# Optimization experiments

Measured on AMD Instinct MI355X. Metric: run time of the kernel, lower is better.

## Reference

```python
import jax, jax.numpy as jnp
import numpy as np

N = 50000      # nodes
E = 800000     # edges
FIN = 128      # num_feature
EDIM = 16      # edge_dim
OUT = 64       # out_dim (per-head channels; concat=False averages heads)
H = 4          # heads
SCALE = 1.0 / float(np.sqrt(OUT))


def _layernorm(h, g, b):
    mu = h.mean(-1, keepdims=True)
    var = ((h - mu) ** 2).mean(-1, keepdims=True)
    return (h - mu) * jax.lax.rsqrt(var + 1e-5) * g + b


def _tconv(x, src, dst, ea, Wq, bq, Wk, bk, Wv, bv, We, Ws, bs):
    # PyG TransformerConv, concat=False, root_weight=True, eval mode (no dropout)
    n = x.shape[0]
    q = (x @ Wq + bq).reshape(n, H, OUT)[dst]   # [E,H,D] query at destination
    k = (x @ Wk + bk).reshape(n, H, OUT)[src]   # [E,H,D] key at source
    v = (x @ Wv + bv).reshape(n, H, OUT)[src]   # [E,H,D] value at source
    e = (ea @ We).reshape(-1, H, OUT)           # [E,H,D] edge embedding (no bias)
    logits = jnp.einsum('ehd,ehd->eh', q, k + e) * SCALE   # [E,H]
    # segment softmax over incoming edges of each destination node
    m = jax.lax.stop_gradient(jax.ops.segment_max(logits, dst, num_segments=n))
    a = jnp.exp(logits - m[dst])
    s = jax.ops.segment_sum(a, dst, num_segments=n)
    alpha = a / s[dst]                                     # [E,H]
    agg = jax.ops.segment_sum((v + e) * alpha[..., None], dst, num_segments=n)  # [N,H,D]
    return agg.mean(axis=1) + x @ Ws + bs      # concat=False -> head mean; + skip


def _forward(x, src, dst, ea, p1, p2, p3, g, b):
    h = x
    for p in (p1, p2, p3):
        h = jax.nn.gelu(_layernorm(_tconv(h, src, dst, ea, *p), g, b), approximate=False)
    return h


def setup_inputs() -> dict:
    key = jax.random.key(0)
    ks = iter(jax.random.split(key, 64))
    def nrm(shp, s=0.05):
        return jax.random.normal(next(ks), shp, jnp.float32) * s
    inp = {
        'x': nrm((N, FIN), 1.0),
        'edge_index': jax.random.randint(next(ks), (2, E), 0, N),
        'edge_attr': nrm((E, EDIM), 1.0),
    }
    for l, fin in ((1, FIN), (2, OUT), (3, OUT)):
        inp[f'Wq{l}'] = nrm((fin, H * OUT)); inp[f'bq{l}'] = jnp.zeros((H * OUT,), jnp.float32)
        inp[f'Wk{l}'] = nrm((fin, H * OUT)); inp[f'bk{l}'] = jnp.zeros((H * OUT,), jnp.float32)
        inp[f'Wv{l}'] = nrm((fin, H * OUT)); inp[f'bv{l}'] = jnp.zeros((H * OUT,), jnp.float32)
        inp[f'We{l}'] = nrm((EDIM, H * OUT))
        inp[f'Ws{l}'] = nrm((fin, OUT)); inp[f'bs{l}'] = jnp.zeros((OUT,), jnp.float32)
    inp['ln_g'] = jnp.ones((OUT,), jnp.float32)
    inp['ln_b'] = jnp.zeros((OUT,), jnp.float32)
    return inp


def reference(x, edge_index, edge_attr,
              Wq1, bq1, Wk1, bk1, Wv1, bv1, We1, Ws1, bs1,
              Wq2, bq2, Wk2, bk2, Wv2, bv2, We2, Ws2, bs2,
              Wq3, bq3, Wk3, bk3, Wv3, bv3, We3, Ws3, bs3,
              ln_g, ln_b):
    src, dst = edge_index[0], edge_index[1]
    p1 = (Wq1, bq1, Wk1, bk1, Wv1, bv1, We1, Ws1, bs1)
    p2 = (Wq2, bq2, Wk2, bk2, Wv2, bv2, We2, Ws2, bs2)
    p3 = (Wq3, bq3, Wk3, bk3, Wv3, bv3, We3, Ws3, bs3)
    return _forward(x, src, dst, edge_attr, p1, p2, p3, ln_g, ln_b)
```

## Files before the change

### kernel.cpp

```cpp
#include <hip/hip_runtime.h>
#include <hip/hip_bf16.h>
#include <math.h>

#define NNODES 50000
#define NEDGES 800000
#define HD     256
#define CW     384
#define NTOT   896
#define QS     0.18033688011112042f

typedef __hip_bfloat16 bf16;
typedef unsigned short u16;
typedef unsigned char  u8;
typedef unsigned int   u32;
typedef __attribute__((ext_vector_type(8))) short bf16x8;
typedef __attribute__((ext_vector_type(4))) float f32x4;
typedef __attribute__((ext_vector_type(2))) float f32x2;

__device__ __forceinline__ float lo16f(u32 u) { return __uint_as_float(u << 16); }
__device__ __forceinline__ float hi16f(u32 u) { return __uint_as_float(u & 0xFFFF0000u); }
__device__ __forceinline__ short f2s(float v) { __hip_bfloat16 h = __float2bfloat16(v); return *(short*)&h; }

__device__ __forceinline__ void gload_lds16(const void* g, void* l) {
    __builtin_amdgcn_global_load_lds(
        (const __attribute__((address_space(1))) void*)g,
        (__attribute__((address_space(3))) void*)l, 16, 0, 0);
}

template<int CTRL>
__device__ __forceinline__ float dppadd(float x) {
    int t = __builtin_amdgcn_update_dpp(0, __float_as_int(x), CTRL, 0xF, 0xF, true);
    return x + __int_as_float(t);
}

__global__ void hist_kernel(const int* __restrict__ dst, int* __restrict__ deg, int E) {
    int e = blockIdx.x * 256 + threadIdx.x;
    if (e < E) atomicAdd(&deg[dst[e]], 1);
}

__global__ void scanA(const int* __restrict__ deg, int* __restrict__ locincl,
                      int* __restrict__ blocksum, int n) {
    int tid = threadIdx.x;
    int i = blockIdx.x * 256 + tid;
    int v = (i < n) ? deg[i] : 0;
    int lane = tid & 63, w = tid >> 6;
    int s = v;
    #pragma unroll
    for (int off = 1; off < 64; off <<= 1) {
        int t = __shfl_up(s, off);
        if (lane >= off) s += t;
    }
    __shared__ int wsum[4];
    if (lane == 63) wsum[w] = s;
    __syncthreads();
    for (int ww = 0; ww < w; ww++) s += wsum[ww];
    if (i < n) locincl[i] = s;
    if (tid == 255) blocksum[blockIdx.x] = s;
}

__global__ void scanB(const int* __restrict__ blocksum, int* __restrict__ blockoff,
                      int nb, int* __restrict__ rowptr, int n) {
    int tid = threadIdx.x;
    int v = (tid < nb) ? blocksum[tid] : 0;
    int lane = tid & 63, w = tid >> 6;
    int s = v;
    #pragma unroll
    for (int off = 1; off < 64; off <<= 1) {
        int t = __shfl_up(s, off);
        if (lane >= off) s += t;
    }
    __shared__ int wsum[4];
    if (lane == 63) wsum[w] = s;
    __syncthreads();
    for (int ww = 0; ww < w; ww++) s += wsum[ww];
    if (tid < nb) blockoff[tid] = s - v;
    if (tid == 255) rowptr[n] = s;
}

__global__ void scanC(const int* __restrict__ deg, const int* __restrict__ locincl,
                      const int* __restrict__ blockoff,
                      int* __restrict__ rowptr, int* __restrict__ cursor, int n) {
    int i = blockIdx.x * 256 + threadIdx.x;
    if (i < n) {
        int ex = locincl[i] - deg[i] + blockoff[blockIdx.x];
        rowptr[i] = ex;
        cursor[i] = ex;
    }
}

__global__ void scatter_kernel(const int* __restrict__ src, const int* __restrict__ dst,
                               int* __restrict__ cursor,
                               int* __restrict__ csr_src, int* __restrict__ csr_eid, int E) {
    int e = blockIdx.x * 256 + threadIdx.x;
    if (e < E) {
        int d = dst[e];
        int p = atomicAdd(&cursor[d], 1);
        csr_src[p] = src[e];
        csr_eid[p] = e;
    }
}

__global__ void eperm(const int* __restrict__ csr_eid, const float* __restrict__ eattr,
                      u16* __restrict__ eattr_c) {
    int g = blockIdx.x * 256 + threadIdx.x;
    int p = g >> 2, part = g & 3;
    int eid = csr_eid[p];
    float4 v = *(const float4*)((const u8*)eattr + (size_t)eid * 64 + part * 16);
    union { u16 s[4]; uint2 u; } t;
    t.s[0] = (u16)f2s(v.x); t.s[1] = (u16)f2s(v.y); t.s[2] = (u16)f2s(v.z); t.s[3] = (u16)f2s(v.w);
    *(uint2*)((u8*)eattr_c + (size_t)p * 32 + part * 8) = t.u;
}

__global__ void xcast(const float* __restrict__ x, u16* __restrict__ xb) {
    int i = blockIdx.x * 256 + threadIdx.x;
    const float4* p = (const float4*)(x + (size_t)i * 8);
    float4 a = p[0], b = p[1];
    union { u16 s[8]; uint4 u; } t;
    t.s[0] = (u16)f2s(a.x); t.s[1] = (u16)f2s(a.y); t.s[2] = (u16)f2s(a.z); t.s[3] = (u16)f2s(a.w);
    t.s[4] = (u16)f2s(b.x); t.s[5] = (u16)f2s(b.y); t.s[6] = (u16)f2s(b.z); t.s[7] = (u16)f2s(b.w);
    *(uint4*)(xb + (size_t)i * 8) = t.u;
}

__global__ void pack_all(const float* __restrict__ Wq, const float* __restrict__ bq,
                         const float* __restrict__ Wk, const float* __restrict__ bk,
                         const float* __restrict__ Wv, const float* __restrict__ bv,
                         const float* __restrict__ We,
                         const float* __restrict__ Ws, const float* __restrict__ bs,
                         bf16* __restrict__ Wc, float* __restrict__ b, int K) {
    int n = blockIdx.x, c = threadIdx.x;
    float v, bb;
    if (n < 256)      { v = Wq[(size_t)c * 256 + n] * QS;    bb = bq[n] * QS; }
    else if (n < 320) {
        int t = n - 256, h = t >> 4, j = t & 15;
        float s = 0.f, sb = 0.f;
        #pragma unroll 8
        for (int d = 0; d < 64; d++) {
            float wv = We[j * HD + h * 64 + d];
            s += Wq[(size_t)c * 256 + h * 64 + d] * wv;
            sb += bq[h * 64 + d] * wv;
        }
        v = s * QS; bb = sb * QS;
    }
    else if (n < 384) { v = Ws[(size_t)c * 64  + (n - 320)]; bb = bs[n - 320]; }
    else if (n < 640) { v = Wv[(size_t)c * 256 + (n - 384)]; bb = bv[n - 384]; }
    else              { v = Wk[(size_t)c * 256 + (n - 640)]; bb = bk[n - 640]; }
    Wc[(size_t)n * K + c] = __float2bfloat16(v);
    if (c == 0) b[n] = bb;
}

template<int K>
__global__ void __launch_bounds__(256) gemm_v4(
    const u16* __restrict__ A, const bf16* __restrict__ Wc, const float* __restrict__ bias,
    bf16* __restrict__ comb, u8* __restrict__ kv)
{
    constexpr int KS    = K / 32;
    constexpr int ITERS = 4;
    constexpr int ROWB  = K * 2;
    constexpr int TILEB = 64 * ROWB;
    constexpr int WSEG  = TILEB / 4;
    constexpr int NINST = WSEG / 1024;
    __shared__ __align__(16) u8 Ab[2][TILEB];
    __shared__ __align__(16) u8 TrB[4][2560];
    int tid = threadIdx.x, w = tid >> 6, lane = tid & 63;
    int cl = lane & 15, aq = lane >> 4;
    int chunk = blockIdx.x;
    int slab = blockIdx.y * (64 * ITERS);
    u8* myT = TrB[w];

    bf16x8 bfr[4][KS];
    #pragma unroll
    for (int t = 0; t < 4; t++)
        #pragma unroll
        for (int ks = 0; ks < KS; ks++)
            bfr[t][ks] = *(const bf16x8*)((const u16*)Wc +
                         (size_t)(chunk * 64 + t * 16 + cl) * K + ks * 32 + aq * 8);

    float4 bv[4];
    #pragma unroll
    for (int t = 0; t < 4; t++) bv[t] = *(const float4*)&bias[chunk * 64 + t * 16 + aq * 4];

    auto STAGE = [&](int b, int it) {
        int m0 = slab + it * 64;
        #pragma unroll
        for (int i = 0; i < NINST; i++) {
            int off = w * WSEG + i * 1024;
            int rowbase = off / ROWB;
            int row, gran;
            if constexpr (K == 64) { row = rowbase + (lane >> 3); gran = lane & 7;  }
            else                   { row = rowbase + (lane >> 4); gran = lane & 15; }
            int gr = m0 + row; if (gr >= NNODES) gr = NNODES - 1;
            int sg = gran ^ (row & 7);
            gload_lds16((const u8*)A + (size_t)gr * ROWB + sg * 16, Ab[b] + off);
        }
    };

    STAGE(0, 0);
    __syncthreads();
    int cur = 0;
    #pragma unroll
    for (int it = 0; it < ITERS; it++) {
        if (it + 1 < ITERS) STAGE(cur ^ 1, it + 1);

        int rowt = w * 16 + cl;
        bf16x8 a[KS];
        #pragma unroll
        for (int ks = 0; ks < KS; ks++)
            a[ks] = *(const bf16x8*)&Ab[cur][rowt * ROWB + (((ks * 4 + aq) ^ (rowt & 7)) << 4)];

        f32x4 acc[4] = {};
        #pragma unroll
        for (int t = 0; t < 4; t++)
            #pragma unroll
            for (int ks = 0; ks < KS; ks++)
                acc[t] = __builtin_amdgcn_mfma_f32_16x16x32_bf16(bfr[t][ks], a[ks], acc[t], 0, 0, 0);

        if (chunk < 10) {
            #pragma unroll
            for (int t = 0; t < 4; t++) {
                u32 lo = (u32)(u16)f2s(acc[t][0] + bv[t].x) | ((u32)(u16)f2s(acc[t][1] + bv[t].y) << 16);
                u32 hi = (u32)(u16)f2s(acc[t][2] + bv[t].z) | ((u32)(u16)f2s(acc[t][3] + bv[t].w) << 16);
                *(uint2*)(myT + cl * 160 + t * 32 + aq * 8) = make_uint2(lo, hi);
            }
            #pragma unroll
            for (int i = 0; i < 2; i++) {
                int r = i * 8 + (lane >> 3);
                uint4 vv = *(const uint4*)(myT + r * 160 + (lane & 7) * 16);
                int gr = slab + it * 64 + w * 16 + r;
                if (gr < NNODES) {
                    u8* dst = (chunk < 6) ? (u8*)comb + (size_t)gr * (CW * 2) + chunk * 128
                                          : kv + (size_t)gr * 768 + (chunk - 6) * 128;
                    *(uint4*)(dst + (lane & 7) * 16) = vv;
                }
            }
        } else {
            #pragma unroll
            for (int t = 0; t < 4; t++) {
                u32 pk = __builtin_amdgcn_cvt_pk_fp8_f32(acc[t][0] + bv[t].x, acc[t][1] + bv[t].y, 0, false);
                pk = __builtin_amdgcn_cvt_pk_fp8_f32(acc[t][2] + bv[t].z, acc[t][3] + bv[t].w, pk, true);
                *(u32*)(myT + cl * 80 + (t * 4 + aq) * 4) = pk;
            }
            {
                int r = lane >> 2;
                uint4 vv = *(const uint4*)(myT + r * 80 + (lane & 3) * 16);
                int gr = slab + it * 64 + w * 16 + r;
                if (gr < NNODES)
                    *(uint4*)(kv + (size_t)gr * 768 + 512 + (chunk - 10) * 64 + (lane & 3) * 16) = vv;
            }
        }
        __syncthreads();
        cur ^= 1;
    }
}

__global__ void __launch_bounds__(256) node_fused(
    const int* __restrict__ rowptr, const int* __restrict__ csr_src,
    const u16* __restrict__ eattr_c, const u16* __restrict__ comb,
    const u8* __restrict__ kv,
    const float* __restrict__ We, const float* __restrict__ lng, const float* __restrict__ lnb,
    bf16* __restrict__ outB, float* __restrict__ outF)
{
    int tid = threadIdx.x, w = tid >> 6, lane = tid & 63;
    int n = blockIdx.x * 4 + w;
    int hg = lane >> 4, j16 = lane & 15, coff = 4 * lane;
    __shared__ float sAV[4][256];
    __shared__ float sAE[4][64];

    const u16* crow = comb + (size_t)n * CW;
    uint2 qv = *(const uint2*)(crow + coff);
    float qf0 = lo16f(qv.x), qf1 = hi16f(qv.x), qf2 = lo16f(qv.y), qf3 = hi16f(qv.y);
    float qwe_r = __uint_as_float((u32)crow[256 + lane] << 16);

    int e0 = __builtin_amdgcn_readfirstlane(rowptr[n]);
    int e1 = __builtin_amdgcn_readfirstlane(rowptr[n + 1]);

    float ss = 0.f, av0 = 0.f, av1 = 0.f, av2 = 0.f, av3 = 0.f, ae = 0.f;
    u32 vo = (u32)coff * 2u;
    u32 eo = (u32)j16 * 2u;

    auto EDGE = [&](int sm, int pos) {
        u32 s = (u32)__builtin_amdgcn_readfirstlane(sm);
        const u8* kvp = kv + (size_t)s * 768u;
        uint2 vw = *(const uint2*)(kvp + vo);
        u32   kw = *(const u32*)  (kvp + 512u + (u32)coff);
        float ea = lo16f((u32)*(const u16*)((const u8*)eattr_c + (size_t)(u32)pos * 32u + eo));
        f32x2 k01 = __builtin_amdgcn_cvt_pk_f32_fp8(kw, false);
        f32x2 k23 = __builtin_amdgcn_cvt_pk_f32_fp8(kw, true);
        float part = qf0 * k01[0] + qf1 * k01[1] + qf2 * k23[0] + qf3 * k23[1] + qwe_r * ea;
        part = dppadd<0xB1>(part);
        part = dppadd<0x4E>(part);
        part = dppadd<0x141>(part);
        part = dppadd<0x140>(part);
        float alpha = __builtin_amdgcn_exp2f(part);
        ss += alpha;
        ae += alpha * ea;
        av0 += alpha * lo16f(vw.x); av1 += alpha * hi16f(vw.x);
        av2 += alpha * lo16f(vw.y); av3 += alpha * hi16f(vw.y);
    };

    const int* cs = csr_src;
    int i = e0;
    int m0 = 0, m1 = 0, m2 = 0, m3 = 0, m4 = 0, m5 = 0, m6 = 0, m7 = 0;
    if (i + 7 < e1) {
        m0 = cs[i];     m1 = cs[i + 1]; m2 = cs[i + 2]; m3 = cs[i + 3];
        m4 = cs[i + 4]; m5 = cs[i + 5]; m6 = cs[i + 6]; m7 = cs[i + 7];
    }
    for (; i + 15 < e1; i += 8) {
        int n0 = cs[i + 8],  n1 = cs[i + 9],  n2 = cs[i + 10], n3 = cs[i + 11];
        int n4 = cs[i + 12], n5 = cs[i + 13], n6 = cs[i + 14], n7 = cs[i + 15];
        EDGE(m0, i);     EDGE(m1, i + 1); EDGE(m2, i + 2); EDGE(m3, i + 3);
        EDGE(m4, i + 4); EDGE(m5, i + 5); EDGE(m6, i + 6); EDGE(m7, i + 7);
        m0 = n0; m1 = n1; m2 = n2; m3 = n3; m4 = n4; m5 = n5; m6 = n6; m7 = n7;
    }
    if (i + 7 < e1) {
        EDGE(m0, i);     EDGE(m1, i + 1); EDGE(m2, i + 2); EDGE(m3, i + 3);
        EDGE(m4, i + 4); EDGE(m5, i + 5); EDGE(m6, i + 6); EDGE(m7, i + 7);
        i += 8;
    }
    for (; i < e1; ++i) EDGE(cs[i], i);

    float inv = (ss > 0.f) ? 1.f / ss : 0.f;
    *(float4*)&sAV[w][coff] = make_float4(av0 * inv, av1 * inv, av2 * inv, av3 * inv);
    sAE[w][lane] = ae * inv;

    int d = lane;
    float val = 0.f;
    #pragma unroll
    for (int h = 0; h < 4; h++) {
        float xv = sAV[w][h * 64 + d];
        #pragma unroll
        for (int j = 0; j < 16; j++) xv += sAE[w][h * 16 + j] * We[j * HD + h * 64 + d];
        val += xv;
    }
    val = val * 0.25f + __uint_as_float((u32)crow[320 + d] << 16);

    float m = val;
    #pragma unroll
    for (int off = 1; off < 64; off <<= 1) m += __shfl_xor(m, off);
    m *= (1.f / 64.f);
    float diff = val - m;
    float vr = diff * diff;
    #pragma unroll
    for (int off = 1; off < 64; off <<= 1) vr += __shfl_xor(vr, off);
    vr *= (1.f / 64.f);
    float y = diff * rsqrtf(vr + 1e-5f) * lng[d] + lnb[d];
    float ge = 0.5f * y * (1.f + erff(y * 0.70710678118654752f));
    if (outF) outF[(size_t)n * 64 + d] = ge;
    else      outB[(size_t)n * 64 + d] = __float2bfloat16(ge);
}

extern "C" void kernel_launch(void* const* d_in, const int* in_sizes, int n_in,
                              void* d_out, int out_size, void* d_ws, size_t ws_size,
                              hipStream_t stream)
{
    const float* x     = (const float*)d_in[0];
    const int*   eidx  = (const int*)d_in[1];
    const float* eattr = (const float*)d_in[2];
    struct P { const float *Wq,*bq,*Wk,*bk,*Wv,*bv,*We,*Ws,*bs; };
    P p[3];
    for (int l = 0; l < 3; l++) {
        int base = 3 + l * 9;
        p[l].Wq = (const float*)d_in[base + 0]; p[l].bq = (const float*)d_in[base + 1];
        p[l].Wk = (const float*)d_in[base + 2]; p[l].bk = (const float*)d_in[base + 3];
        p[l].Wv = (const float*)d_in[base + 4]; p[l].bv = (const float*)d_in[base + 5];
        p[l].We = (const float*)d_in[base + 6];
        p[l].Ws = (const float*)d_in[base + 7]; p[l].bs = (const float*)d_in[base + 8];
    }
    const float* lng = (const float*)d_in[30];
    const float* lnb = (const float*)d_in[31];

    char* ws = (char*)d_ws;
    size_t off = 0;
    auto alloc = [&](size_t bytes) { void* pp = ws + off; off += (bytes + 255) & ~(size_t)255; return pp; };
    int*   rowptr   = (int*)  alloc((NNODES + 1) * 4);
    int*   cursor   = (int*)  alloc(NNODES * 4);
    int*   deg      = (int*)  alloc(NNODES * 4);
    int*   blocksum = (int*)  alloc(256 * 4);
    int*   blockoff = (int*)  alloc(256 * 4);
    int*   csr_src  = (int*)  alloc((size_t)NEDGES * 4);
    int*   csr_eid  = (int*)  alloc((size_t)NEDGES * 4);
    u16*   eattr_c  = (u16*)  alloc((size_t)NEDGES * 16 * 2);
    bf16*  hbuf     = (bf16*) alloc((size_t)NNODES * 64 * 2);
    u16*   xb       = (u16*)  alloc((size_t)NNODES * 128 * 2);
    bf16*  comb     = (bf16*) alloc((size_t)NNODES * CW * 2);
    u8*    kv       = (u8*)   alloc((size_t)NNODES * 768);
    bf16*  Wc       = (bf16*) alloc((size_t)NTOT * 128 * 2);
    float* b896     = (float*)alloc(NTOT * 4);
    (void)ws_size;

    const int* srcArr = eidx;
    const int* dstArr = eidx + NEDGES;

    int NB = (NNODES + 255) / 256;
    (void)hipMemsetAsync(deg, 0, NNODES * 4, stream);
    hist_kernel<<<(NEDGES + 255) / 256, 256, 0, stream>>>(dstArr, deg, NEDGES);
    scanA<<<NB, 256, 0, stream>>>(deg, cursor, blocksum, NNODES);
    scanB<<<1, 256, 0, stream>>>(blocksum, blockoff, NB, rowptr, NNODES);
    scanC<<<NB, 256, 0, stream>>>(deg, cursor, blockoff, rowptr, cursor, NNODES);
    scatter_kernel<<<(NEDGES + 255) / 256, 256, 0, stream>>>(srcArr, dstArr, cursor, csr_src, csr_eid, NEDGES);
    eperm<<<(4 * NEDGES) / 256, 256, 0, stream>>>(csr_eid, eattr, eattr_c);
    xcast<<<(NNODES * 128 / 8 + 255) / 256, 256, 0, stream>>>(x, xb);

    int NBY = (NNODES + 255) / 256;
    int fins[3] = {128, 64, 64};

    const u16* hin = xb;
    for (int l = 0; l < 3; l++) {
        int FIN = fins[l];
        pack_all<<<NTOT, FIN, 0, stream>>>(p[l].Wq, p[l].bq, p[l].Wk, p[l].bk,
                                           p[l].Wv, p[l].bv, p[l].We, p[l].Ws, p[l].bs,
                                           Wc, b896, FIN);
        if (l == 0) gemm_v4<128><<<dim3(14, NBY), 256, 0, stream>>>(hin, Wc, b896, comb, kv);
        else        gemm_v4<64> <<<dim3(14, NBY), 256, 0, stream>>>(hin, Wc, b896, comb, kv);
        node_fused<<<NNODES / 4, 256, 0, stream>>>(rowptr, csr_src, eattr_c, (const u16*)comb,
            kv, p[l].We, lng, lnb,
            (l == 2) ? nullptr : hbuf, (l == 2) ? (float*)d_out : nullptr);
        hin = (const u16*)hbuf;
    }
}
```

Measured before the change: 662.1 us.

## Use persistent dynamic node scheduling and fuse edge-attr permute into scatter

The node aggregation kernel becomes a persistent grid of 2048 blocks whose waves claim pairs of nodes from a global atomic counter, one counter per layer, instead of one wave per node from a static grid. This is meant to balance the irregular per-node degree and cut wave launch overhead. Separately, the eperm kernel and the csr_eid buffer are removed: the scatter kernel now converts each edge's attributes to bf16 and writes them straight to their CSR slot. That saves a launch and an index round trip, but each thread now does a 32-byte scattered write, and the work queue adds atomic contention.

Result: slower. 1.560 ms (+135.6%).

```diff
diff --git a/kernel.cpp b/kernel.cpp
--- a/kernel.cpp
+++ b/kernel.cpp
@@ -89,26 +89,24 @@
 }
 
 __global__ void scatter_kernel(const int* __restrict__ src, const int* __restrict__ dst,
-                               int* __restrict__ cursor,
-                               int* __restrict__ csr_src, int* __restrict__ csr_eid, int E) {
+                               int* __restrict__ cursor, int* __restrict__ csr_src,
+                               const float* __restrict__ eattr, u16* __restrict__ eattr_c, int E) {
     int e = blockIdx.x * 256 + threadIdx.x;
     if (e < E) {
         int d = dst[e];
         int p = atomicAdd(&cursor[d], 1);
         csr_src[p] = src[e];
-        csr_eid[p] = e;
-    }
-}
-
-__global__ void eperm(const int* __restrict__ csr_eid, const float* __restrict__ eattr,
-                      u16* __restrict__ eattr_c) {
-    int g = blockIdx.x * 256 + threadIdx.x;
-    int p = g >> 2, part = g & 3;
-    int eid = csr_eid[p];
-    float4 v = *(const float4*)((const u8*)eattr + (size_t)eid * 64 + part * 16);
-    union { u16 s[4]; uint2 u; } t;
-    t.s[0] = (u16)f2s(v.x); t.s[1] = (u16)f2s(v.y); t.s[2] = (u16)f2s(v.z); t.s[3] = (u16)f2s(v.w);
-    *(uint2*)((u8*)eattr_c + (size_t)p * 32 + part * 8) = t.u;
+        const float4* er = (const float4*)(eattr + (size_t)e * 16);
+        float4 a = er[0], b = er[1], c = er[2], f = er[3];
+        union { u16 s[16]; uint4 u[2]; } t;
+        t.s[0]  = (u16)f2s(a.x); t.s[1]  = (u16)f2s(a.y); t.s[2]  = (u16)f2s(a.z); t.s[3]  = (u16)f2s(a.w);
+        t.s[4]  = (u16)f2s(b.x); t.s[5]  = (u16)f2s(b.y); t.s[6]  = (u16)f2s(b.z); t.s[7]  = (u16)f2s(b.w);
+        t.s[8]  = (u16)f2s(c.x); t.s[9]  = (u16)f2s(c.y); t.s[10] = (u16)f2s(c.z); t.s[11] = (u16)f2s(c.w);
+        t.s[12] = (u16)f2s(f.x); t.s[13] = (u16)f2s(f.y); t.s[14] = (u16)f2s(f.z); t.s[15] = (u16)f2s(f.w);
+        uint4* dstp = (uint4*)((u8*)eattr_c + (size_t)p * 32);
+        dstp[0] = t.u[0];
+        dstp[1] = t.u[1];
+    }
 }
 
 __global__ void xcast(const float* __restrict__ x, u16* __restrict__ xb) {
@@ -253,6 +251,7 @@
 }
 
 __global__ void __launch_bounds__(256) node_fused(
+    int* __restrict__ ctr,
     const int* __restrict__ rowptr, const int* __restrict__ csr_src,
     const u16* __restrict__ eattr_c, const u16* __restrict__ comb,
     const u8* __restrict__ kv,
@@ -260,92 +259,102 @@
     bf16* __restrict__ outB, float* __restrict__ outF)
 {
     int tid = threadIdx.x, w = tid >> 6, lane = tid & 63;
-    int n = blockIdx.x * 4 + w;
     int hg = lane >> 4, j16 = lane & 15, coff = 4 * lane;
     __shared__ float sAV[4][256];
     __shared__ float sAE[4][64];
 
-    const u16* crow = comb + (size_t)n * CW;
-    uint2 qv = *(const uint2*)(crow + coff);
-    float qf0 = lo16f(qv.x), qf1 = hi16f(qv.x), qf2 = lo16f(qv.y), qf3 = hi16f(qv.y);
-    float qwe_r = __uint_as_float((u32)crow[256 + lane] << 16);
-
-    int e0 = __builtin_amdgcn_readfirstlane(rowptr[n]);
-    int e1 = __builtin_amdgcn_readfirstlane(rowptr[n + 1]);
-
-    float ss = 0.f, av0 = 0.f, av1 = 0.f, av2 = 0.f, av3 = 0.f, ae = 0.f;
     u32 vo = (u32)coff * 2u;
     u32 eo = (u32)j16 * 2u;
-
-    auto EDGE = [&](int sm, int pos) {
-        u32 s = (u32)__builtin_amdgcn_readfirstlane(sm);
-        const u8* kvp = kv + (size_t)s * 768u;
-        uint2 vw = *(const uint2*)(kvp + vo);
-        u32   kw = *(const u32*)  (kvp + 512u + (u32)coff);
-        float ea = lo16f((u32)*(const u16*)((const u8*)eattr_c + (size_t)(u32)pos * 32u + eo));
-        f32x2 k01 = __builtin_amdgcn_cvt_pk_f32_fp8(kw, false);
-        f32x2 k23 = __builtin_amdgcn_cvt_pk_f32_fp8(kw, true);
-        float part = qf0 * k01[0] + qf1 * k01[1] + qf2 * k23[0] + qf3 * k23[1] + qwe_r * ea;
-        part = dppadd<0xB1>(part);
-        part = dppadd<0x4E>(part);
-        part = dppadd<0x141>(part);
-        part = dppadd<0x140>(part);
-        float alpha = __builtin_amdgcn_exp2f(part);
-        ss += alpha;
-        ae += alpha * ea;
-        av0 += alpha * lo16f(vw.x); av1 += alpha * hi16f(vw.x);
-        av2 += alpha * lo16f(vw.y); av3 += alpha * hi16f(vw.y);
-    };
-
     const int* cs = csr_src;
-    int i = e0;
-    int m0 = 0, m1 = 0, m2 = 0, m3 = 0, m4 = 0, m5 = 0, m6 = 0, m7 = 0;
-    if (i + 7 < e1) {
-        m0 = cs[i];     m1 = cs[i + 1]; m2 = cs[i + 2]; m3 = cs[i + 3];
-        m4 = cs[i + 4]; m5 = cs[i + 5]; m6 = cs[i + 6]; m7 = cs[i + 7];
-    }
-    for (; i + 15 < e1; i += 8) {
-        int n0 = cs[i + 8],  n1 = cs[i + 9],  n2 = cs[i + 10], n3 = cs[i + 11];
-        int n4 = cs[i + 12], n5 = cs[i + 13], n6 = cs[i + 14], n7 = cs[i + 15];
-        EDGE(m0, i);     EDGE(m1, i + 1); EDGE(m2, i + 2); EDGE(m3, i + 3);
-        EDGE(m4, i + 4); EDGE(m5, i + 5); EDGE(m6, i + 6); EDGE(m7, i + 7);
-        m0 = n0; m1 = n1; m2 = n2; m3 = n3; m4 = n4; m5 = n5; m6 = n6; m7 = n7;
-    }
-    if (i + 7 < e1) {
-        EDGE(m0, i);     EDGE(m1, i + 1); EDGE(m2, i + 2); EDGE(m3, i + 3);
-        EDGE(m4, i + 4); EDGE(m5, i + 5); EDGE(m6, i + 6); EDGE(m7, i + 7);
-        i += 8;
-    }
-    for (; i < e1; ++i) EDGE(cs[i], i);
-
-    float inv = (ss > 0.f) ? 1.f / ss : 0.f;
-    *(float4*)&sAV[w][coff] = make_float4(av0 * inv, av1 * inv, av2 * inv, av3 * inv);
-    sAE[w][lane] = ae * inv;
-
-    int d = lane;
-    float val = 0.f;
-    #pragma unroll
-    for (int h = 0; h < 4; h++) {
-        float xv = sAV[w][h * 64 + d];
-        #pragma unroll
-        for (int j = 0; j < 16; j++) xv += sAE[w][h * 16 + j] * We[j * HD + h * 64 + d];
-        val += xv;
-    }
-    val = val * 0.25f + __uint_as_float((u32)crow[320 + d] << 16);
-
-    float m = val;
-    #pragma unroll
-    for (int off = 1; off < 64; off <<= 1) m += __shfl_xor(m, off);
-    m *= (1.f / 64.f);
-    float diff = val - m;
-    float vr = diff * diff;
-    #pragma unroll
-    for (int off = 1; off < 64; off <<= 1) vr += __shfl_xor(vr, off);
-    vr *= (1.f / 64.f);
-    float y = diff * rsqrtf(vr + 1e-5f) * lng[d] + lnb[d];
-    float ge = 0.5f * y * (1.f + erff(y * 0.70710678118654752f));
-    if (outF) outF[(size_t)n * 64 + d] = ge;
-    else      outB[(size_t)n * 64 + d] = __float2bfloat16(ge);
+
+    for (;;) {
+        int base = 0;
+        if (lane == 0) base = atomicAdd(ctr, 2);
+        base = __shfl(base, 0);
+        if (base >= NNODES) break;
+        int nend = base + 2; if (nend > NNODES) nend = NNODES;
+
+        for (int n = base; n < nend; n++) {
+            const u16* crow = comb + (size_t)n * CW;
+            uint2 qv = *(const uint2*)(crow + coff);
+            float qf0 = lo16f(qv.x), qf1 = hi16f(qv.x), qf2 = lo16f(qv.y), qf3 = hi16f(qv.y);
+            float qwe_r = __uint_as_float((u32)crow[256 + lane] << 16);
+
+            int e0 = __builtin_amdgcn_readfirstlane(rowptr[n]);
+            int e1 = __builtin_amdgcn_readfirstlane(rowptr[n + 1]);
+
+            float ss = 0.f, av0 = 0.f, av1 = 0.f, av2 = 0.f, av3 = 0.f, ae = 0.f;
+
+            auto EDGE = [&](int sm, int pos) {
+                u32 s = (u32)__builtin_amdgcn_readfirstlane(sm);
+                const u8* kvp = kv + (size_t)s * 768u;
+                uint2 vw = *(const uint2*)(kvp + vo);
+                u32   kw = *(const u32*)  (kvp + 512u + (u32)coff);
+                float ea = lo16f((u32)*(const u16*)((const u8*)eattr_c + (size_t)(u32)pos * 32u + eo));
+                f32x2 k01 = __builtin_amdgcn_cvt_pk_f32_fp8(kw, false);
+                f32x2 k23 = __builtin_amdgcn_cvt_pk_f32_fp8(kw, true);
+                float part = qf0 * k01[0] + qf1 * k01[1] + qf2 * k23[0] + qf3 * k23[1] + qwe_r * ea;
+                part = dppadd<0xB1>(part);
+                part = dppadd<0x4E>(part);
+                part = dppadd<0x141>(part);
+                part = dppadd<0x140>(part);
+                float alpha = __builtin_amdgcn_exp2f(part);
+                ss += alpha;
+                ae += alpha * ea;
+                av0 += alpha * lo16f(vw.x); av1 += alpha * hi16f(vw.x);
+                av2 += alpha * lo16f(vw.y); av3 += alpha * hi16f(vw.y);
+            };
+
+            int i = e0;
+            int m0 = 0, m1 = 0, m2 = 0, m3 = 0, m4 = 0, m5 = 0, m6 = 0, m7 = 0;
+            if (i + 7 < e1) {
+                m0 = cs[i];     m1 = cs[i + 1]; m2 = cs[i + 2]; m3 = cs[i + 3];
+                m4 = cs[i + 4]; m5 = cs[i + 5]; m6 = cs[i + 6]; m7 = cs[i + 7];
+            }
+            for (; i + 15 < e1; i += 8) {
+                int n0 = cs[i + 8],  n1 = cs[i + 9],  n2 = cs[i + 10], n3 = cs[i + 11];
+                int n4 = cs[i + 12], n5 = cs[i + 13], n6 = cs[i + 14], n7 = cs[i + 15];
+                EDGE(m0, i);     EDGE(m1, i + 1); EDGE(m2, i + 2); EDGE(m3, i + 3);
+                EDGE(m4, i + 4); EDGE(m5, i + 5); EDGE(m6, i + 6); EDGE(m7, i + 7);
+                m0 = n0; m1 = n1; m2 = n2; m3 = n3; m4 = n4; m5 = n5; m6 = n6; m7 = n7;
+            }
+            if (i + 7 < e1) {
+                EDGE(m0, i);     EDGE(m1, i + 1); EDGE(m2, i + 2); EDGE(m3, i + 3);
+                EDGE(m4, i + 4); EDGE(m5, i + 5); EDGE(m6, i + 6); EDGE(m7, i + 7);
+                i += 8;
+            }
+            for (; i < e1; ++i) EDGE(cs[i], i);
+
+            float inv = (ss > 0.f) ? 1.f / ss : 0.f;
+            *(float4*)&sAV[w][coff] = make_float4(av0 * inv, av1 * inv, av2 * inv, av3 * inv);
+            sAE[w][lane] = ae * inv;
+
+            int d = lane;
+            float val = 0.f;
+            #pragma unroll
+            for (int h = 0; h < 4; h++) {
+                float xv = sAV[w][h * 64 + d];
+                #pragma unroll
+                for (int j = 0; j < 16; j++) xv += sAE[w][h * 16 + j] * We[j * HD + h * 64 + d];
+                val += xv;
+            }
+            val = val * 0.25f + __uint_as_float((u32)crow[320 + d] << 16);
+
+            float m = val;
+            #pragma unroll
+            for (int off = 1; off < 64; off <<= 1) m += __shfl_xor(m, off);
+            m *= (1.f / 64.f);
+            float diff = val - m;
+            float vr = diff * diff;
+            #pragma unroll
+            for (int off = 1; off < 64; off <<= 1) vr += __shfl_xor(vr, off);
+            vr *= (1.f / 64.f);
+            float y = diff * rsqrtf(vr + 1e-5f) * lng[d] + lnb[d];
+            float ge = 0.5f * y * (1.f + erff(y * 0.70710678118654752f));
+            if (outF) outF[(size_t)n * 64 + d] = ge;
+            else      outB[(size_t)n * 64 + d] = __float2bfloat16(ge);
+        }
+    }
 }
 
 extern "C" void kernel_launch(void* const* d_in, const int* in_sizes, int n_in,
@@ -376,8 +385,8 @@
     int*   deg      = (int*)  alloc(NNODES * 4);
     int*   blocksum = (int*)  alloc(256 * 4);
     int*   blockoff = (int*)  alloc(256 * 4);
+    int*   nctr     = (int*)  alloc(8 * 4);
     int*   csr_src  = (int*)  alloc((size_t)NEDGES * 4);
-    int*   csr_eid  = (int*)  alloc((size_t)NEDGES * 4);
     u16*   eattr_c  = (u16*)  alloc((size_t)NEDGES * 16 * 2);
     bf16*  hbuf     = (bf16*) alloc((size_t)NNODES * 64 * 2);
     u16*   xb       = (u16*)  alloc((size_t)NNODES * 128 * 2);
@@ -392,12 +401,13 @@
 
     int NB = (NNODES + 255) / 256;
     (void)hipMemsetAsync(deg, 0, NNODES * 4, stream);
+    (void)hipMemsetAsync(nctr, 0, 32, stream);
     hist_kernel<<<(NEDGES + 255) / 256, 256, 0, stream>>>(dstArr, deg, NEDGES);
     scanA<<<NB, 256, 0, stream>>>(deg, cursor, blocksum, NNODES);
     scanB<<<1, 256, 0, stream>>>(blocksum, blockoff, NB, rowptr, NNODES);
     scanC<<<NB, 256, 0, stream>>>(deg, cursor, blockoff, rowptr, cursor, NNODES);
-    scatter_kernel<<<(NEDGES + 255) / 256, 256, 0, stream>>>(srcArr, dstArr, cursor, csr_src, csr_eid, NEDGES);
-    eperm<<<(4 * NEDGES) / 256, 256, 0, stream>>>(csr_eid, eattr, eattr_c);
+    scatter_kernel<<<(NEDGES + 255) / 256, 256, 0, stream>>>(srcArr, dstArr, cursor,
+                                                             csr_src, eattr, eattr_c, NEDGES);
     xcast<<<(NNODES * 128 / 8 + 255) / 256, 256, 0, stream>>>(x, xb);
 
     int NBY = (NNODES + 255) / 256;
@@ -411,8 +421,8 @@
                                            Wc, b896, FIN);
         if (l == 0) gemm_v4<128><<<dim3(14, NBY), 256, 0, stream>>>(hin, Wc, b896, comb, kv);
         else        gemm_v4<64> <<<dim3(14, NBY), 256, 0, stream>>>(hin, Wc, b896, comb, kv);
-        node_fused<<<NNODES / 4, 256, 0, stream>>>(rowptr, csr_src, eattr_c, (const u16*)comb,
-            kv, p[l].We, lng, lnb,
+        node_fused<<<2048, 256, 0, stream>>>(nctr + l, rowptr, csr_src, eattr_c,
+            (const u16*)comb, kv, p[l].We, lng, lnb,
             (l == 2) ? nullptr : hbuf, (l == 2) ? (float*)d_out : nullptr);
         hin = (const u16*)hbuf;
     }
```
